# Kernel tuning notes

Hardware: AMD Instinct MI355X
Metric: run time of the kernel (lower is better)

The kernel has to match this reference:

```python
import math
import jax, jax.numpy as jnp
import numpy as np

N, S, D = 1024, 256, 256
C, R, CLASSES = 256, 64, 1000


def setup_inputs() -> dict:
    key = jax.random.key(0)
    ks = jax.random.split(key, 10)
    inv_sqrt_d = 1.0 / math.sqrt(D)
    return {
        "q": jax.random.normal(ks[0], (N, D), dtype=jnp.float32),
        "K": jax.random.normal(ks[1], (N, S, D), dtype=jnp.float32),
        "V": jax.random.normal(ks[2], (N, S, D), dtype=jnp.float32),
        "codebook": jax.random.normal(ks[3], (C, D), dtype=jnp.float32) * inv_sqrt_d,
        "residual_codebook": jax.random.normal(ks[4], (R, D), dtype=jnp.float32) * inv_sqrt_d,
        "Wq": jax.random.normal(ks[5], (D, D), dtype=jnp.float32) * inv_sqrt_d,
        "residual_logit": jnp.zeros((), dtype=jnp.float32),
        "Wc": jax.random.normal(ks[6], (CLASSES, D), dtype=jnp.float32) * inv_sqrt_d,
        "bc": jnp.zeros((CLASSES,), dtype=jnp.float32),
        "Wr": jax.random.normal(ks[7], (D, D), dtype=jnp.float32) * inv_sqrt_d,
        "br": jnp.zeros((D,), dtype=jnp.float32),
    }


def reference(q, K, V, codebook, residual_codebook, Wq, residual_logit, Wc, bc, Wr, br):
    scale = math.sqrt(q.shape[-1])
    q_proj = q @ Wq.T  # [N,D]

    # --- base codebook pass ---
    code_weights = jax.nn.softmax(jnp.einsum('nd,cd->nc', q_proj, codebook) / scale, axis=-1)
    slot_code_weights = jax.nn.softmax(jnp.einsum('nsd,cd->nsc', K, codebook) / scale, axis=-1)
    slot_code_summaries = jnp.einsum('nsc,nsd->ncd', slot_code_weights, V)
    base_summary = jnp.einsum('nc,ncd->nd', code_weights, slot_code_summaries)
    base_weights = jnp.einsum('nc,nsc->ns', code_weights, slot_code_weights)

    # --- residual quantization pass ---
    query_residual = q_proj - code_weights @ codebook
    slot_residual = K - jnp.einsum('nsc,cd->nsd', slot_code_weights, codebook)
    residual_code_weights = jax.nn.softmax(
        jnp.einsum('nd,rd->nr', query_residual, residual_codebook) / scale, axis=-1)
    residual_slot_code_weights = jax.nn.softmax(
        jnp.einsum('nsd,rd->nsr', slot_residual, residual_codebook) / scale, axis=-1)
    residual_slot_summaries = jnp.einsum('nsr,nsd->nrd', residual_slot_code_weights, V)
    residual_summary = jnp.einsum('nr,nrd->nd', residual_code_weights, residual_slot_summaries)
    residual_weights = jnp.einsum('nr,nsr->ns', residual_code_weights, residual_slot_code_weights)

    gate = jax.nn.sigmoid(residual_logit)
    summary = base_summary + gate * residual_summary
    effective_weights = (base_weights + gate * residual_weights) / (1.0 + gate)

    logits = summary @ Wc.T + bc
    recon = summary @ Wr.T + br
    return (logits, recon, effective_weights)
```

## Files before the change

### kernel.cpp

```cpp
#include <hip/hip_runtime.h>
#include <hip/hip_bf16.h>
#include <math.h>

#define N_   1024
#define S_   256
#define D_   256
#define C_   256
#define R_   64
#define CLS_ 1000
#define INV16 0.0625f

typedef unsigned short ushortT;
typedef unsigned int uint32;
typedef short bf8 __attribute__((ext_vector_type(8)));
typedef float f4 __attribute__((ext_vector_type(4)));

static __device__ __forceinline__ float bf2f(uint32 u){
  return __uint_as_float(u << 16);
}
static __device__ __forceinline__ ushortT f2bf(float f){
  uint32 x = __float_as_uint(f);
  uint32 r = x + 0x7FFFu + ((x >> 16) & 1u);
  return (ushortT)(r >> 16);
}
static __device__ __forceinline__ uint32 packbf(float a, float b){
  return ((uint32)f2bf(b) << 16) | (uint32)f2bf(a);
}
static __device__ __forceinline__ float wred_max(float v){
  for (int o = 32; o; o >>= 1) v = fmaxf(v, __shfl_xor(v, o));
  return v;
}
static __device__ __forceinline__ float wred_sum(float v){
  for (int o = 32; o; o >>= 1) v += __shfl_xor(v, o);
  return v;
}
static __device__ __forceinline__ int swz(int row, int colbyte){
  return row*512 + ((colbyte & ~15) ^ ((row & 7) << 4)) + (colbyte & 15);
}
static __device__ __forceinline__ int pkidx(int row, int col, int nfrag){
  int ks = col >> 5, hi = (col >> 3) & 3, e = col & 7;
  int frag = row >> 4, l15p = row & 15;
  return ((ks*nfrag + frag)*64 + hi*16 + l15p)*8 + e;
}

__global__ __launch_bounds__(256) void k0(const float* __restrict__ cb,
    const float* __restrict__ rcb, const float* __restrict__ Wc,
    const float* __restrict__ Wr, ushortT* __restrict__ a1pk,
    ushortT* __restrict__ Wcr_bf)
{
  int t = blockIdx.x*256 + threadIdx.x;
  int stride = gridDim.x*256;
  for (int e = t; e < (C_ + R_)*D_; e += stride){
    int row = e >> 8, col = e & 255;
    float v = (row < C_) ? cb[e] : rcb[e - C_*D_];
    a1pk[pkidx(row, col, 20)] = f2bf(v);
  }
  for (int e = t; e < CLS_*D_; e += stride) Wcr_bf[e] = f2bf(Wc[e]);
  for (int e = t; e < D_*D_; e += stride)  Wcr_bf[CLS_*D_ + e] = f2bf(Wr[e]);
  for (int e = t; e < 24*D_; e += stride)  Wcr_bf[1256*D_ + e] = 0;
}

__global__ __launch_bounds__(256) void k0m(const float* __restrict__ cb,
    const float* __restrict__ rcb, float* __restrict__ MT_f32,
    ushortT* __restrict__ mtpk)
{
  __shared__ float rl[D_];
  int r = blockIdx.x;
  int t = threadIdx.x;
  rl[t] = rcb[r*D_ + t];
  __syncthreads();
  float acc = 0.f;
  const float* crow = cb + t*D_;
  #pragma unroll 8
  for (int k = 0; k < D_; k += 4){
    float4 w = *(const float4*)(crow + k);
    acc += w.x*rl[k] + w.y*rl[k+1] + w.z*rl[k+2] + w.w*rl[k+3];
  }
  MT_f32[r*C_ + t] = acc;
  mtpk[pkidx(r, t, 4)] = f2bf(acc);
}

__global__ __launch_bounds__(256) void k1(const float* __restrict__ q,
    const float* __restrict__ cb, const float* __restrict__ rcb,
    const float* __restrict__ Wq, const float* __restrict__ MT_f32,
    float* __restrict__ cw_ws, float* __restrict__ rcw_ws)
{
  __shared__ float qv[D_], qp[D_], red[8], redB[8], cwl[C_];
  int n = blockIdx.x, t = threadIdx.x;
  qv[t] = q[n*D_ + t];
  __syncthreads();
  {
    float acc = 0.f;
    const float* wrow = Wq + t*D_;
    #pragma unroll 8
    for (int k = 0; k < D_; k += 4){
      float4 w = *(const float4*)(wrow + k);
      acc += qv[k]*w.x + qv[k+1]*w.y + qv[k+2]*w.z + qv[k+3]*w.w;
    }
    qp[t] = acc;
  }
  __syncthreads();
  float L = 0.f;
  {
    const float* crow = cb + t*D_;
    #pragma unroll 8
    for (int k = 0; k < D_; k += 4){
      float4 w = *(const float4*)(crow + k);
      L += qp[k]*w.x + qp[k+1]*w.y + qp[k+2]*w.z + qp[k+3]*w.w;
    }
    L *= INV16;
  }
  float m = wred_max(L);
  if ((t & 63) == 0) red[t >> 6] = m;
  __syncthreads();
  m = fmaxf(fmaxf(red[0], red[1]), fmaxf(red[2], red[3]));
  float e = __expf(L - m);
  float s = wred_sum(e);
  if ((t & 63) == 0) redB[t >> 6] = s;
  __syncthreads();
  s = redB[0] + redB[1] + redB[2] + redB[3];
  float w = e / s;
  cwl[t] = w;
  cw_ws[n*C_ + t] = w;
  __syncthreads();
  if (t < R_){
    float qdot = 0.f, mdot = 0.f;
    const float* rrow = rcb + t*D_;
    const float* mrow = MT_f32 + t*C_;
    #pragma unroll 8
    for (int k = 0; k < D_; k += 4){
      float4 wv = *(const float4*)(rrow + k);
      qdot += qp[k]*wv.x + qp[k+1]*wv.y + qp[k+2]*wv.z + qp[k+3]*wv.w;
      float4 mv = *(const float4*)(mrow + k);
      mdot += cwl[k]*mv.x + cwl[k+1]*mv.y + cwl[k+2]*mv.z + cwl[k+3]*mv.w;
    }
    float Lr = (qdot - mdot) * INV16;
    float mr = wred_max(Lr);
    float er = __expf(Lr - mr);
    float sr = wred_sum(er);
    rcw_ws[n*R_ + t] = er / sr;
  }
}

__global__ __launch_bounds__(256, 3) void k2(const float* __restrict__ Kt,
    const float* __restrict__ Vt, const ushortT* __restrict__ a1pk,
    const ushortT* __restrict__ mtpk, const float* __restrict__ cw_ws,
    const float* __restrict__ rcw_ws, const float* __restrict__ rlogit,
    float* __restrict__ sum_ws, float* __restrict__ out_ew)
{
  __shared__ __align__(16) ushortT KW[64*256];
  __shared__ float redS[4][64], redW[4][64];
  __shared__ float cwl[C_], rcwl[R_];

  int bx  = blockIdx.x;
  int n   = bx >> 2;
  int s0  = (bx & 3) * 64;
  int tid = threadIdx.x;
  int lane = tid & 63, w = tid >> 6;
  int l15 = lane & 15, l4 = lane >> 4;
  int sabs = w*16 + l15;
  float gate  = 1.f / (1.f + __expf(-rlogit[0]));
  float inv1g = 1.f / (1.f + gate);

  const float* Kn = Kt + (size_t)n * S_ * D_ + (size_t)s0 * D_;
  const float* Vn = Vt + (size_t)n * S_ * D_ + (size_t)s0 * D_;

  if (tid < C_) cwl[tid]  = cw_ws[n*C_ + tid];
  if (tid < R_) rcwl[tid] = rcw_ws[n*R_ + tid];

  #pragma unroll
  for (int j = 0; j < 8; j++){
    int ch = tid + j*256;
    int row = ch >> 5, blk = ch & 31;
    const float* src = Kn + row*D_ + blk*8;
    float4 a = *(const float4*)src;
    float4 b = *(const float4*)(src + 4);
    uint4 wv = {packbf(a.x,a.y), packbf(a.z,a.w), packbf(b.x,b.y), packbf(b.z,b.w)};
    *(uint4*)((char*)KW + swz(row, blk*16)) = wv;
  }
  __syncthreads();

  float cw_r[16];
  #pragma unroll
  for (int f = 0; f < 4; f++)
    #pragma unroll
    for (int rg = 0; rg < 4; rg++)
      cw_r[f*4+rg] = cwl[(w + 4*f)*16 + l4*4 + rg];
  float rcw_r[4];
  #pragma unroll
  for (int rg = 0; rg < 4; rg++) rcw_r[rg] = rcwl[w*16 + l4*4 + rg];

  const ushortT* a1w = a1pk + (size_t)(w*64 + lane)*8;
  bf8 bnx[5];
  #pragma unroll
  for (int f = 0; f < 5; f++)
    bnx[f] = *(const bf8*)(a1w + (size_t)(4*f)*512);
  f4 acc[5][4];
  #pragma unroll
  for (int f = 0; f < 5; f++)
    #pragma unroll
    for (int sj = 0; sj < 4; sj++) acc[f][sj] = (f4)0.f;
  #pragma unroll
  for (int ks = 0; ks < 8; ks++){
    bf8 bcur[5];
    #pragma unroll
    for (int f = 0; f < 5; f++) bcur[f] = bnx[f];
    if (ks < 7){
      #pragma unroll
      for (int f = 0; f < 5; f++)
        bnx[f] = *(const bf8*)(a1w + (size_t)((ks+1)*20 + 4*f)*512);
    }
    bf8 kf[4];
    #pragma unroll
    for (int sj = 0; sj < 4; sj++)
      kf[sj] = *(const bf8*)((const char*)KW + swz(sj*16 + l15, ks*64 + l4*16));
    #pragma unroll
    for (int f = 0; f < 5; f++)
      #pragma unroll
      for (int sj = 0; sj < 4; sj++)
        acc[f][sj] = __builtin_amdgcn_mfma_f32_16x16x32_bf16(bcur[f], kf[sj], acc[f][sj], 0, 0, 0);
  }

  float se[4] = {0,0,0,0}, sb[4] = {0,0,0,0};
  #pragma unroll
  for (int f = 0; f < 4; f++)
    #pragma unroll
    for (int sj = 0; sj < 4; sj++)
      #pragma unroll
      for (int rg = 0; rg < 4; rg++){
        float e = __expf(acc[f][sj][rg] * INV16);
        acc[f][sj][rg] = e;
        se[sj] += e;
        sb[sj] += e * cw_r[f*4+rg];
      }
  #pragma unroll
  for (int sj = 0; sj < 4; sj++){
    se[sj] += __shfl_xor(se[sj], 16); se[sj] += __shfl_xor(se[sj], 32);
    sb[sj] += __shfl_xor(sb[sj], 16); sb[sj] += __shfl_xor(sb[sj], 32);
  }
  if (l4 == 0){
    #pragma unroll
    for (int sj = 0; sj < 4; sj++){
      redS[w][sj*16 + l15] = se[sj];
      redW[w][sj*16 + l15] = sb[sj];
    }
  }
  __syncthreads();
  float rcp[4];
  #pragma unroll
  for (int sj = 0; sj < 4; sj++){
    int s_ = sj*16 + l15;
    rcp[sj] = 1.f / (redS[0][s_] + redS[1][s_] + redS[2][s_] + redS[3][s_]);
  }
  float bw_loc;
  {
    float sS = redS[0][sabs] + redS[1][sabs] + redS[2][sabs] + redS[3][sabs];
    float sW = redW[0][sabs] + redW[1][sabs] + redW[2][sabs] + redW[3][sabs];
    bw_loc = sW / sS;
  }
  #pragma unroll
  for (int f = 0; f < 4; f++){
    int cbyte = ((w + 4*f)*16 + l4*4) * 2;
    #pragma unroll
    for (int sj = 0; sj < 4; sj++){
      int s_ = sj*16 + l15;
      float r = rcp[sj];
      *(uint32*)((char*)KW + swz(s_, cbyte))     = packbf(acc[f][sj][0]*r, acc[f][sj][1]*r);
      *(uint32*)((char*)KW + swz(s_, cbyte + 4)) = packbf(acc[f][sj][2]*r, acc[f][sj][3]*r);
    }
  }
  __syncthreads();

  const ushortT* mtw = mtpk + (size_t)(w*64 + lane)*8;
  bf8 mnx = *(const bf8*)(mtw);
  f4 wmacc[4];
  #pragma unroll
  for (int sj = 0; sj < 4; sj++) wmacc[sj] = (f4)0.f;
  #pragma unroll
  for (int ks = 0; ks < 8; ks++){
    bf8 a = mnx;
    if (ks < 7) mnx = *(const bf8*)(mtw + (size_t)((ks+1)*4)*512);
    #pragma unroll
    for (int sj = 0; sj < 4; sj++){
      bf8 b = *(const bf8*)((const char*)KW + swz(sj*16 + l15, ks*64 + l4*16));
      wmacc[sj] = __builtin_amdgcn_mfma_f32_16x16x32_bf16(a, b, wmacc[sj], 0, 0, 0);
    }
  }

  float se3[4] = {0,0,0,0}, sc3[4] = {0,0,0,0};
  #pragma unroll
  for (int sj = 0; sj < 4; sj++)
    #pragma unroll
    for (int rg = 0; rg < 4; rg++){
      float e = __expf((acc[4][sj][rg] - wmacc[sj][rg]) * INV16);
      se3[sj] += e;
      sc3[sj] += e * rcw_r[rg];
    }
  #pragma unroll
  for (int sj = 0; sj < 4; sj++){
    se3[sj] += __shfl_xor(se3[sj], 16); se3[sj] += __shfl_xor(se3[sj], 32);
    sc3[sj] += __shfl_xor(sc3[sj], 16); sc3[sj] += __shfl_xor(sc3[sj], 32);
  }
  if (l4 == 0){
    #pragma unroll
    for (int sj = 0; sj < 4; sj++){
      redS[w][sj*16 + l15] = se3[sj];
      redW[w][sj*16 + l15] = sc3[sj];
    }
  }
  float4 vld[16];
  {
    const float* vp = Vn + (size_t)(w*16)*D_ + lane*4;
    #pragma unroll
    for (int j = 0; j < 16; j++)
      vld[j] = *(const float4*)(vp + (size_t)j*D_);
  }
  __syncthreads();
  float comb;
  {
    float sS = redS[0][sabs] + redS[1][sabs] + redS[2][sabs] + redS[3][sabs];
    float sW = redW[0][sabs] + redW[1][sabs] + redW[2][sabs] + redW[3][sabs];
    comb = bw_loc + gate * (sW / sS);
    if (l4 == 0) out_ew[n*S_ + s0 + sabs] = comb * inv1g;
  }

  {
    float4 sacc = {0.f, 0.f, 0.f, 0.f};
    #pragma unroll
    for (int j = 0; j < 16; j++){
      float cj = __shfl(comb, j);
      float4 v = vld[j];
      sacc.x = fmaf(cj, v.x, sacc.x); sacc.y = fmaf(cj, v.y, sacc.y);
      sacc.z = fmaf(cj, v.z, sacc.z); sacc.w = fmaf(cj, v.w, sacc.w);
    }
    float* dst = sum_ws + (size_t)n*D_ + lane*4;
    atomicAdd(dst + 0, sacc.x);
    atomicAdd(dst + 1, sacc.y);
    atomicAdd(dst + 2, sacc.z);
    atomicAdd(dst + 3, sacc.w);
  }
}

__global__ __launch_bounds__(256) void k3(const float* __restrict__ sum_ws,
    const ushortT* __restrict__ Wcr_bf, const float* __restrict__ bc,
    const float* __restrict__ br, float* __restrict__ out)
{
  __shared__ __align__(16) ushortT Stile[64*256];
  int bx = blockIdx.x;
  int ot = bx >> 4;
  int nt = bx & 15;
  int tid = threadIdx.x;
  int lane = tid & 63, wid = tid >> 6;
  int l15 = lane & 15, l4 = lane >> 4;

  const float* Sp = sum_ws + (size_t)nt*64*D_;
  #pragma unroll
  for (int j = 0; j < 8; j++){
    int ch = tid + j*256;
    int row = ch >> 5, blk = ch & 31;
    const float* src = Sp + row*D_ + blk*8;
    float4 a = *(const float4*)src;
    float4 b = *(const float4*)(src + 4);
    uint4 wv = {packbf(a.x,a.y), packbf(a.z,a.w), packbf(b.x,b.y), packbf(b.z,b.w)};
    *(uint4*)((char*)Stile + swz(row, blk*16)) = wv;
  }
  __syncthreads();

  int o0 = ot*64 + wid*16;
  const ushortT* Ap = Wcr_bf + (size_t)(o0 + l15)*D_ + l4*8;
  f4 acc[4];
  #pragma unroll
  for (int j = 0; j < 4; j++) acc[j] = (f4)0.f;
  #pragma unroll
  for (int k = 0; k < 8; k++){
    bf8 a = *(const bf8*)(Ap + k*32);
    #pragma unroll
    for (int nj = 0; nj < 4; nj++){
      bf8 b = *(const bf8*)((const char*)Stile + swz(nj*16 + l15, k*64 + l4*16));
      acc[nj] = __builtin_amdgcn_mfma_f32_16x16x32_bf16(a, b, acc[nj], 0, 0, 0);
    }
  }
  int obase = o0 + l4*4;
  if (obase < 1256){
    float4 bias;
    if (obase < CLS_) bias = *(const float4*)(bc + obase);
    else              bias = *(const float4*)(br + (obase - CLS_));
    #pragma unroll
    for (int nj = 0; nj < 4; nj++){
      int nn = nt*64 + nj*16 + l15;
      float4 v = {acc[nj][0]+bias.x, acc[nj][1]+bias.y, acc[nj][2]+bias.z, acc[nj][3]+bias.w};
      if (obase < CLS_) *(float4*)(out + (size_t)nn*CLS_ + obase) = v;
      else              *(float4*)(out + (size_t)N_*CLS_ + (size_t)nn*D_ + (obase - CLS_)) = v;
    }
  }
}

extern "C" void kernel_launch(void* const* d_in, const int* in_sizes, int n_in,
                              void* d_out, int out_size, void* d_ws, size_t ws_size,
                              hipStream_t stream)
{
  const float* q    = (const float*)d_in[0];
  const float* Kt   = (const float*)d_in[1];
  const float* Vt   = (const float*)d_in[2];
  const float* cb   = (const float*)d_in[3];
  const float* rcb  = (const float*)d_in[4];
  const float* Wq   = (const float*)d_in[5];
  const float* rlg  = (const float*)d_in[6];
  const float* Wc   = (const float*)d_in[7];
  const float* bc   = (const float*)d_in[8];
  const float* Wr   = (const float*)d_in[9];
  const float* br   = (const float*)d_in[10];
  float* out = (float*)d_out;
  float* ws  = (float*)d_ws;

  float* cw_ws  = ws;
  float* rcw_ws = ws + 262144;
  float* sum_ws = ws + 327680;
  float* MT_f32 = ws + 589824;
  ushortT* a1pk   = (ushortT*)(ws + 606208);
  ushortT* mtpk   = a1pk + (C_ + R_)*D_;
  ushortT* Wcr_bf = mtpk + R_*C_;

  float* out_logits = out;
  float* out_ew     = out + (size_t)N_*CLS_ + (size_t)N_*D_;

  hipMemsetAsync(sum_ws, 0, (size_t)N_*D_*sizeof(float), stream);
  k0 <<<128,  256, 0, stream>>>(cb, rcb, Wc, Wr, a1pk, Wcr_bf);
  k0m<<<R_,   256, 0, stream>>>(cb, rcb, MT_f32, mtpk);
  k1 <<<N_,   256, 0, stream>>>(q, cb, rcb, Wq, MT_f32, cw_ws, rcw_ws);
  k2 <<<N_*4, 256, 0, stream>>>(Kt, Vt, a1pk, mtpk, cw_ws, rcw_ws, rlg,
                                sum_ws, out_ew);
  k3 <<<320,  256, 0, stream>>>(sum_ws, Wcr_bf, bc, br, out_logits);
}
```

Baseline: 258.4 us.

## Restructure k2 so each wave owns 32 slots with register-resident K and no block syncs

The main fused kernel changes from 64 slots per block split across waves by code column to 32 slots per wave, with each wave computing all 320 code logits for its own slots. K fragments now live in registers rather than a swizzled shared tile, so the softmax reductions become wave-local shuffles and all __syncthreads barriers disappear. The grid is halved, the occupancy hint is dropped, and normalization by the row sum is applied after the second MFMA pass instead of before it. In exchange, register pressure rises sharply (80 accumulator vectors plus 20 prefetched B fragments), which may lower occupancy or cause spills, and every wave now streams the full codebook operand itself.

```diff
diff --git a/kernel.cpp b/kernel.cpp
--- a/kernel.cpp
+++ b/kernel.cpp
@@ -142,203 +142,166 @@
   }
 }
 
-__global__ __launch_bounds__(256, 3) void k2(const float* __restrict__ Kt,
+__global__ __launch_bounds__(256) void k2(const float* __restrict__ Kt,
     const float* __restrict__ Vt, const ushortT* __restrict__ a1pk,
     const ushortT* __restrict__ mtpk, const float* __restrict__ cw_ws,
     const float* __restrict__ rcw_ws, const float* __restrict__ rlogit,
     float* __restrict__ sum_ws, float* __restrict__ out_ew)
 {
-  __shared__ __align__(16) ushortT KW[64*256];
-  __shared__ float redS[4][64], redW[4][64];
-  __shared__ float cwl[C_], rcwl[R_];
+  __shared__ __align__(16) ushortT Wl[4][32][264];
 
   int bx  = blockIdx.x;
-  int n   = bx >> 2;
-  int s0  = (bx & 3) * 64;
+  int n   = bx >> 1;
   int tid = threadIdx.x;
   int lane = tid & 63, w = tid >> 6;
   int l15 = lane & 15, l4 = lane >> 4;
-  int sabs = w*16 + l15;
+  int s0w = (bx & 1)*128 + w*32;
   float gate  = 1.f / (1.f + __expf(-rlogit[0]));
   float inv1g = 1.f / (1.f + gate);
 
-  const float* Kn = Kt + (size_t)n * S_ * D_ + (size_t)s0 * D_;
-  const float* Vn = Vt + (size_t)n * S_ * D_ + (size_t)s0 * D_;
-
-  if (tid < C_) cwl[tid]  = cw_ws[n*C_ + tid];
-  if (tid < R_) rcwl[tid] = rcw_ws[n*R_ + tid];
-
-  #pragma unroll
-  for (int j = 0; j < 8; j++){
-    int ch = tid + j*256;
-    int row = ch >> 5, blk = ch & 31;
-    const float* src = Kn + row*D_ + blk*8;
-    float4 a = *(const float4*)src;
-    float4 b = *(const float4*)(src + 4);
-    uint4 wv = {packbf(a.x,a.y), packbf(a.z,a.w), packbf(b.x,b.y), packbf(b.z,b.w)};
-    *(uint4*)((char*)KW + swz(row, blk*16)) = wv;
-  }
-  __syncthreads();
-
-  float cw_r[16];
-  #pragma unroll
-  for (int f = 0; f < 4; f++)
-    #pragma unroll
-    for (int rg = 0; rg < 4; rg++)
-      cw_r[f*4+rg] = cwl[(w + 4*f)*16 + l4*4 + rg];
-  float rcw_r[4];
-  #pragma unroll
-  for (int rg = 0; rg < 4; rg++) rcw_r[rg] = rcwl[w*16 + l4*4 + rg];
-
-  const ushortT* a1w = a1pk + (size_t)(w*64 + lane)*8;
-  bf8 bnx[5];
-  #pragma unroll
-  for (int f = 0; f < 5; f++)
-    bnx[f] = *(const bf8*)(a1w + (size_t)(4*f)*512);
-  f4 acc[5][4];
-  #pragma unroll
-  for (int f = 0; f < 5; f++)
-    #pragma unroll
-    for (int sj = 0; sj < 4; sj++) acc[f][sj] = (f4)0.f;
+  const float* Kn = Kt + (size_t)n*S_*D_ + (size_t)s0w*D_;
+  const float* Vn = Vt + (size_t)n*S_*D_ + (size_t)s0w*D_;
+
+  bf8 kreg[16];
+  #pragma unroll
+  for (int sh = 0; sh < 2; sh++)
+    #pragma unroll
+    for (int ks = 0; ks < 8; ks++){
+      const float* kp = Kn + (size_t)(sh*16 + l15)*D_ + ks*32 + l4*8;
+      float4 a = *(const float4*)kp;
+      float4 b = *(const float4*)(kp + 4);
+      union { bf8 v; uint32 u[4]; } x;
+      x.u[0] = packbf(a.x, a.y); x.u[1] = packbf(a.z, a.w);
+      x.u[2] = packbf(b.x, b.y); x.u[3] = packbf(b.z, b.w);
+      kreg[sh*8 + ks] = x.v;
+    }
+
+  const ushortT* a1w = a1pk + (size_t)lane*8;
+  bf8 bnx[20];
+  #pragma unroll
+  for (int f = 0; f < 20; f++)
+    bnx[f] = *(const bf8*)(a1w + (size_t)f*512);
+  f4 acc[20][2];
+  #pragma unroll
+  for (int f = 0; f < 20; f++){ acc[f][0] = (f4)0.f; acc[f][1] = (f4)0.f; }
   #pragma unroll
   for (int ks = 0; ks < 8; ks++){
-    bf8 bcur[5];
-    #pragma unroll
-    for (int f = 0; f < 5; f++) bcur[f] = bnx[f];
-    if (ks < 7){
-      #pragma unroll
-      for (int f = 0; f < 5; f++)
-        bnx[f] = *(const bf8*)(a1w + (size_t)((ks+1)*20 + 4*f)*512);
-    }
-    bf8 kf[4];
-    #pragma unroll
-    for (int sj = 0; sj < 4; sj++)
-      kf[sj] = *(const bf8*)((const char*)KW + swz(sj*16 + l15, ks*64 + l4*16));
-    #pragma unroll
-    for (int f = 0; f < 5; f++)
-      #pragma unroll
-      for (int sj = 0; sj < 4; sj++)
-        acc[f][sj] = __builtin_amdgcn_mfma_f32_16x16x32_bf16(bcur[f], kf[sj], acc[f][sj], 0, 0, 0);
-  }
-
-  float se[4] = {0,0,0,0}, sb[4] = {0,0,0,0};
-  #pragma unroll
-  for (int f = 0; f < 4; f++)
-    #pragma unroll
-    for (int sj = 0; sj < 4; sj++)
-      #pragma unroll
-      for (int rg = 0; rg < 4; rg++){
-        float e = __expf(acc[f][sj][rg] * INV16);
-        acc[f][sj][rg] = e;
-        se[sj] += e;
-        sb[sj] += e * cw_r[f*4+rg];
-      }
-  #pragma unroll
-  for (int sj = 0; sj < 4; sj++){
-    se[sj] += __shfl_xor(se[sj], 16); se[sj] += __shfl_xor(se[sj], 32);
-    sb[sj] += __shfl_xor(sb[sj], 16); sb[sj] += __shfl_xor(sb[sj], 32);
-  }
+    #pragma unroll
+    for (int f = 0; f < 20; f++){
+      bf8 a = bnx[f];
+      if (ks < 7) bnx[f] = *(const bf8*)(a1w + (size_t)((ks+1)*20 + f)*512);
+      acc[f][0] = __builtin_amdgcn_mfma_f32_16x16x32_bf16(a, kreg[ks],     acc[f][0], 0, 0, 0);
+      acc[f][1] = __builtin_amdgcn_mfma_f32_16x16x32_bf16(a, kreg[8 + ks], acc[f][1], 0, 0, 0);
+    }
+  }
+
+  float4 cwv[16];
+  #pragma unroll
+  for (int f = 0; f < 16; f++)
+    cwv[f] = *(const float4*)(cw_ws + n*C_ + f*16 + l4*4);
+
+  float se[2] = {0.f, 0.f};
+  #pragma unroll
+  for (int f = 0; f < 16; f++){
+    #pragma unroll
+    for (int sh = 0; sh < 2; sh++){
+      float e0 = __expf(acc[f][sh][0] * INV16);
+      float e1 = __expf(acc[f][sh][1] * INV16);
+      float e2 = __expf(acc[f][sh][2] * INV16);
+      float e3 = __expf(acc[f][sh][3] * INV16);
+      acc[f][sh][0] = e0; acc[f][sh][1] = e1;
+      acc[f][sh][2] = e2; acc[f][sh][3] = e3;
+      se[sh] += (e0 + e1) + (e2 + e3);
+      ushortT* basep = &Wl[w][sh*16 + l15][f*16 + l4*4];
+      *(uint32*)(basep)     = packbf(e0, e1);
+      *(uint32*)(basep + 2) = packbf(e2, e3);
+    }
+  }
+  float sb[2] = {0.f, 0.f};
+  #pragma unroll
+  for (int f = 0; f < 16; f++)
+    #pragma unroll
+    for (int sh = 0; sh < 2; sh++){
+      sb[sh] += acc[f][sh][0]*cwv[f].x + acc[f][sh][1]*cwv[f].y
+              + acc[f][sh][2]*cwv[f].z + acc[f][sh][3]*cwv[f].w;
+    }
+  #pragma unroll
+  for (int sh = 0; sh < 2; sh++){
+    se[sh] += __shfl_xor(se[sh], 16); se[sh] += __shfl_xor(se[sh], 32);
+    sb[sh] += __shfl_xor(sb[sh], 16); sb[sh] += __shfl_xor(sb[sh], 32);
+  }
+  float rcpS0 = 1.f / se[0], rcpS1 = 1.f / se[1];
+  float bw0 = sb[0] * rcpS0, bw1 = sb[1] * rcpS1;
+
+  bf8 mnx[4];
+  #pragma unroll
+  for (int fr = 0; fr < 4; fr++)
+    mnx[fr] = *(const bf8*)(mtpk + (size_t)(fr*64 + lane)*8);
+  f4 wm[4][2];
+  #pragma unroll
+  for (int fr = 0; fr < 4; fr++){ wm[fr][0] = (f4)0.f; wm[fr][1] = (f4)0.f; }
+  #pragma unroll
+  for (int ks = 0; ks < 8; ks++){
+    bf8 wb0 = *(const bf8*)(&Wl[w][     l15][ks*32 + l4*8]);
+    bf8 wb1 = *(const bf8*)(&Wl[w][16 + l15][ks*32 + l4*8]);
+    #pragma unroll
+    for (int fr = 0; fr < 4; fr++){
+      bf8 a = mnx[fr];
+      if (ks < 7) mnx[fr] = *(const bf8*)(mtpk + (size_t)(((ks+1)*4 + fr)*64 + lane)*8);
+      wm[fr][0] = __builtin_amdgcn_mfma_f32_16x16x32_bf16(a, wb0, wm[fr][0], 0, 0, 0);
+      wm[fr][1] = __builtin_amdgcn_mfma_f32_16x16x32_bf16(a, wb1, wm[fr][1], 0, 0, 0);
+    }
+  }
+
+  float4 rcwv[4];
+  #pragma unroll
+  for (int fr = 0; fr < 4; fr++)
+    rcwv[fr] = *(const float4*)(rcw_ws + n*R_ + fr*16 + l4*4);
+  float se3[2] = {0.f, 0.f}, sc3[2] = {0.f, 0.f};
+  #pragma unroll
+  for (int fr = 0; fr < 4; fr++)
+    #pragma unroll
+    for (int sh = 0; sh < 2; sh++){
+      float rc = sh ? rcpS1 : rcpS0;
+      float e0 = __expf((acc[16+fr][sh][0] - wm[fr][sh][0]*rc) * INV16);
+      float e1 = __expf((acc[16+fr][sh][1] - wm[fr][sh][1]*rc) * INV16);
+      float e2 = __expf((acc[16+fr][sh][2] - wm[fr][sh][2]*rc) * INV16);
+      float e3 = __expf((acc[16+fr][sh][3] - wm[fr][sh][3]*rc) * INV16);
+      se3[sh] += (e0 + e1) + (e2 + e3);
+      sc3[sh] += e0*rcwv[fr].x + e1*rcwv[fr].y + e2*rcwv[fr].z + e3*rcwv[fr].w;
+    }
+  #pragma unroll
+  for (int sh = 0; sh < 2; sh++){
+    se3[sh] += __shfl_xor(se3[sh], 16); se3[sh] += __shfl_xor(se3[sh], 32);
+    sc3[sh] += __shfl_xor(sc3[sh], 16); sc3[sh] += __shfl_xor(sc3[sh], 32);
+  }
+  float comb0 = bw0 + gate * (sc3[0] / se3[0]);
+  float comb1 = bw1 + gate * (sc3[1] / se3[1]);
   if (l4 == 0){
-    #pragma unroll
-    for (int sj = 0; sj < 4; sj++){
-      redS[w][sj*16 + l15] = se[sj];
-      redW[w][sj*16 + l15] = sb[sj];
-    }
-  }
-  __syncthreads();
-  float rcp[4];
-  #pragma unroll
-  for (int sj = 0; sj < 4; sj++){
-    int s_ = sj*16 + l15;
-    rcp[sj] = 1.f / (redS[0][s_] + redS[1][s_] + redS[2][s_] + redS[3][s_]);
-  }
-  float bw_loc;
-  {
-    float sS = redS[0][sabs] + redS[1][sabs] + redS[2][sabs] + redS[3][sabs];
-    float sW = redW[0][sabs] + redW[1][sabs] + redW[2][sabs] + redW[3][sabs];
-    bw_loc = sW / sS;
-  }
-  #pragma unroll
-  for (int f = 0; f < 4; f++){
-    int cbyte = ((w + 4*f)*16 + l4*4) * 2;
-    #pragma unroll
-    for (int sj = 0; sj < 4; sj++){
-      int s_ = sj*16 + l15;
-      float r = rcp[sj];
-      *(uint32*)((char*)KW + swz(s_, cbyte))     = packbf(acc[f][sj][0]*r, acc[f][sj][1]*r);
-      *(uint32*)((char*)KW + swz(s_, cbyte + 4)) = packbf(acc[f][sj][2]*r, acc[f][sj][3]*r);
-    }
-  }
-  __syncthreads();
-
-  const ushortT* mtw = mtpk + (size_t)(w*64 + lane)*8;
-  bf8 mnx = *(const bf8*)(mtw);
-  f4 wmacc[4];
-  #pragma unroll
-  for (int sj = 0; sj < 4; sj++) wmacc[sj] = (f4)0.f;
-  #pragma unroll
-  for (int ks = 0; ks < 8; ks++){
-    bf8 a = mnx;
-    if (ks < 7) mnx = *(const bf8*)(mtw + (size_t)((ks+1)*4)*512);
-    #pragma unroll
-    for (int sj = 0; sj < 4; sj++){
-      bf8 b = *(const bf8*)((const char*)KW + swz(sj*16 + l15, ks*64 + l4*16));
-      wmacc[sj] = __builtin_amdgcn_mfma_f32_16x16x32_bf16(a, b, wmacc[sj], 0, 0, 0);
-    }
-  }
-
-  float se3[4] = {0,0,0,0}, sc3[4] = {0,0,0,0};
-  #pragma unroll
-  for (int sj = 0; sj < 4; sj++)
-    #pragma unroll
-    for (int rg = 0; rg < 4; rg++){
-      float e = __expf((acc[4][sj][rg] - wmacc[sj][rg]) * INV16);
-      se3[sj] += e;
-      sc3[sj] += e * rcw_r[rg];
-    }
-  #pragma unroll
-  for (int sj = 0; sj < 4; sj++){
-    se3[sj] += __shfl_xor(se3[sj], 16); se3[sj] += __shfl_xor(se3[sj], 32);
-    sc3[sj] += __shfl_xor(sc3[sj], 16); sc3[sj] += __shfl_xor(sc3[sj], 32);
-  }
-  if (l4 == 0){
-    #pragma unroll
-    for (int sj = 0; sj < 4; sj++){
-      redS[w][sj*16 + l15] = se3[sj];
-      redW[w][sj*16 + l15] = sc3[sj];
-    }
-  }
-  float4 vld[16];
-  {
-    const float* vp = Vn + (size_t)(w*16)*D_ + lane*4;
-    #pragma unroll
-    for (int j = 0; j < 16; j++)
-      vld[j] = *(const float4*)(vp + (size_t)j*D_);
-  }
-  __syncthreads();
-  float comb;
-  {
-    float sS = redS[0][sabs] + redS[1][sabs] + redS[2][sabs] + redS[3][sabs];
-    float sW = redW[0][sabs] + redW[1][sabs] + redW[2][sabs] + redW[3][sabs];
-    comb = bw_loc + gate * (sW / sS);
-    if (l4 == 0) out_ew[n*S_ + s0 + sabs] = comb * inv1g;
-  }
-
-  {
-    float4 sacc = {0.f, 0.f, 0.f, 0.f};
-    #pragma unroll
-    for (int j = 0; j < 16; j++){
-      float cj = __shfl(comb, j);
-      float4 v = vld[j];
-      sacc.x = fmaf(cj, v.x, sacc.x); sacc.y = fmaf(cj, v.y, sacc.y);
-      sacc.z = fmaf(cj, v.z, sacc.z); sacc.w = fmaf(cj, v.w, sacc.w);
-    }
-    float* dst = sum_ws + (size_t)n*D_ + lane*4;
-    atomicAdd(dst + 0, sacc.x);
-    atomicAdd(dst + 1, sacc.y);
-    atomicAdd(dst + 2, sacc.z);
-    atomicAdd(dst + 3, sacc.w);
-  }
+    out_ew[n*S_ + s0w +      l15] = comb0 * inv1g;
+    out_ew[n*S_ + s0w + 16 + l15] = comb1 * inv1g;
+  }
+
+  float4 sacc = {0.f, 0.f, 0.f, 0.f};
+  #pragma unroll
+  for (int jb = 0; jb < 4; jb++){
+    float4 vb[8];
+    #pragma unroll
+    for (int j = 0; j < 8; j++)
+      vb[j] = *(const float4*)(Vn + (size_t)(jb*8 + j)*D_ + lane*4);
+    #pragma unroll
+    for (int j = 0; j < 8; j++){
+      int s = jb*8 + j;
+      float cj = __shfl(s < 16 ? comb0 : comb1, s & 15);
+      sacc.x = fmaf(cj, vb[j].x, sacc.x); sacc.y = fmaf(cj, vb[j].y, sacc.y);
+      sacc.z = fmaf(cj, vb[j].z, sacc.z); sacc.w = fmaf(cj, vb[j].w, sacc.w);
+    }
+  }
+  float* dst = sum_ws + (size_t)n*D_ + lane*4;
+  atomicAdd(dst + 0, sacc.x);
+  atomicAdd(dst + 1, sacc.y);
+  atomicAdd(dst + 2, sacc.z);
+  atomicAdd(dst + 3, sacc.w);
 }
 
 __global__ __launch_bounds__(256) void k3(const float* __restrict__ sum_ws,
@@ -428,7 +391,7 @@
   k0 <<<128,  256, 0, stream>>>(cb, rcb, Wc, Wr, a1pk, Wcr_bf);
   k0m<<<R_,   256, 0, stream>>>(cb, rcb, MT_f32, mtpk);
   k1 <<<N_,   256, 0, stream>>>(q, cb, rcb, Wq, MT_f32, cw_ws, rcw_ws);
-  k2 <<<N_*4, 256, 0, stream>>>(Kt, Vt, a1pk, mtpk, cw_ws, rcw_ws, rlg,
+  k2 <<<N_*2, 256, 0, stream>>>(Kt, Vt, a1pk, mtpk, cw_ws, rcw_ws, rlg,
                                 sum_ws, out_ew);
   k3 <<<320,  256, 0, stream>>>(sum_ws, Wcr_bf, bc, br, out_logits);
 }
```

After: 293.7 us. 1.14x slower.
